# Kernel optimization log

Measured on AMD Instinct MI355X. Metric: run time of the kernel, lower is better.

Reference implementation:

```python
import jax, jax.numpy as jnp
import numpy as np
from jax.scipy.special import logsumexp

B = 2048       # anchors
P = 4          # positives per anchor (constant -> ragged list collapses to [B,P])
D = 256        # embed dim
N_NEG = 32768  # shared negative bank
TEMPERATURE = 0.05
ALPHA = 0.1
EPS = 1e-12    # F.normalize eps


def _l2norm(x):
    n = jnp.sqrt(jnp.sum(x * x, axis=-1, keepdims=True))
    return x / jnp.maximum(n, EPS)


def setup_inputs() -> dict:
    key = jax.random.key(0)
    k1, k2, k3 = jax.random.split(key, 3)
    return {
        "anchor_embeddings": jax.random.normal(k1, (B, D), jnp.float32),
        "positive_embeddings": jax.random.normal(k2, (B * P, D), jnp.float32),
        "negative_embeddings": jax.random.normal(k3, (N_NEG, D), jnp.float32),
        "num_positives_per_anchor": jnp.full((B,), P, dtype=jnp.int32),
    }


def reference(anchor_embeddings, positive_embeddings, negative_embeddings,
              num_positives_per_anchor):
    a = _l2norm(anchor_embeddings)                       # [B, D]
    p = _l2norm(positive_embeddings).reshape(B, P, D)    # [B, P, D]
    n = _l2norm(negative_embeddings)                     # [N, D]

    pos_sim = jnp.einsum("bd,bpd->bp", a, p) / TEMPERATURE   # [B, P]
    neg_sim = jnp.einsum("bd,nd->bn", a, n) / TEMPERATURE    # [B, N]  (dominant traffic)
    neg_lse = logsumexp(neg_sim, axis=1)                     # [B]

    # per-(anchor, positive) CE with label 0 over logits [pos_j, neg_sim_i]:
    # loss = logsumexp([pos_j, neg...]) - pos_j = logaddexp(pos_j, neg_lse_i) - pos_j
    pair_loss = jnp.logaddexp(pos_sim, neg_lse[:, None]) - pos_sim   # [B, P]
    counts = num_positives_per_anchor
    pair_mask = jnp.arange(P)[None, :] < counts[:, None]             # [B, P]
    total = jnp.sum(jnp.where(pair_mask, pair_loss, 0.0))

    # weighted-positive term (only for anchors with num_pos > 1)
    w = jax.nn.softmax(pos_sim, axis=1)                  # [B, P]
    wps = jnp.sum(w * pos_sim, axis=1)                   # [B]
    wloss = jnp.logaddexp(wps, neg_lse) - wps            # [B]
    total = total + ALPHA * jnp.sum(jnp.where(counts > 1, wloss, 0.0))

    return total / B
```

## Files before the change

### kernel.cpp

```cpp
#include <hip/hip_runtime.h>
#include <math.h>

constexpr int   B       = 2048;
constexpr int   P       = 4;
constexpr int   D       = 256;
constexpr int   NNEG    = 32768;
constexpr int   NTILES  = NNEG / 32;
constexpr float TEMP    = 0.05f;
constexpr float ALPHA   = 0.1f;
constexpr float EPS     = 1e-12f;
constexpr float INV_T   = 1.0f / TEMP;
constexpr float SCALE_Q = 28.853900817779268f;

typedef float f32x4 __attribute__((ext_vector_type(4)));
typedef int   i32x8 __attribute__((ext_vector_type(8)));

__device__ inline unsigned short f2bf(float f) {
  unsigned int u = __float_as_uint(f);
  u = (u + 0x7fffu + ((u >> 16) & 1u)) >> 16;
  return (unsigned short)u;
}
__device__ inline float bf2f(unsigned short u) {
  return __uint_as_float((unsigned int)u << 16);
}

__device__ inline float ror16_add(float v) {
  int x;
  x = __builtin_amdgcn_update_dpp(0, __float_as_int(v), 0x121, 0xf, 0xf, true);
  v += __int_as_float(x);
  x = __builtin_amdgcn_update_dpp(0, __float_as_int(v), 0x122, 0xf, 0xf, true);
  v += __int_as_float(x);
  x = __builtin_amdgcn_update_dpp(0, __float_as_int(v), 0x124, 0xf, 0xf, true);
  v += __int_as_float(x);
  x = __builtin_amdgcn_update_dpp(0, __float_as_int(v), 0x128, 0xf, 0xf, true);
  v += __int_as_float(x);
  return v;
}


constexpr int NPANEL = (B + NNEG) / 16;
constexpr int LSTR   = 264;

__global__ __launch_bounds__(256) void prep_kernel(
    const float* __restrict__ a,
    const float* __restrict__ pzx,
    const float* __restrict__ n,
    unsigned char* __restrict__ a_f8,
    unsigned char* __restrict__ n_f8,
    float* __restrict__ pos_sim,
    float* __restrict__ loss_acc,
    unsigned int* __restrict__ ticket) {
  if (blockIdx.x == 0 && threadIdx.x == 0) { *loss_acc = 0.0f; *ticket = 0u; }
  const int id   = blockIdx.x;
  const int tid  = threadIdx.x;
  const int wave = tid >> 6;
  const int lane = tid & 63;

  if (id < NPANEL) {
    __shared__ __align__(16) unsigned short sm[16 * LSTR];
    const bool isA = (id < B / 16);
    const float* src; unsigned char* dst; int prow; float post;
    if (isA) { src = a; dst = a_f8; prow = id;          post = SCALE_Q; }
    else     { src = n; dst = n_f8; prow = id - B / 16; post = 1.0f; }

#pragma unroll
    for (int rr = 0; rr < 4; rr++) {
      const int r = wave * 4 + rr;
      float4 v = ((const float4*)(src + ((size_t)prow * 16 + r) * D))[lane];
      float ss = v.x * v.x + v.y * v.y + v.z * v.z + v.w * v.w;
#pragma unroll
      for (int off = 32; off > 0; off >>= 1) ss += __shfl_xor(ss, off, 64);
      float inv = post / fmaxf(sqrtf(ss), EPS);
      ushort4 o;
      o.x = f2bf(v.x * inv); o.y = f2bf(v.y * inv);
      o.z = f2bf(v.z * inv); o.w = f2bf(v.w * inv);
      *(ushort4*)&sm[r * LSTR + lane * 4] = o;
    }
    __syncthreads();

    const int o = tid * 16;
    int r, k0;
    if (isA) {
      r  = (o >> 4) & 15;
      k0 = (o >> 11) * 128 + ((o >> 8) & 3) * 32 + ((o >> 10) & 1) * 16;
    } else {
      r  = (o >> 5) & 15;
      k0 = (o >> 11) * 128 + ((o >> 9) & 3) * 32 + (o & 16);
    }
    const unsigned short* s1 = &sm[r * LSTR + k0];
    uint4 ov;
    {
      int w0 = __builtin_amdgcn_cvt_pk_fp8_f32(bf2f(s1[0]),  bf2f(s1[1]),  0,  false);
      w0     = __builtin_amdgcn_cvt_pk_fp8_f32(bf2f(s1[2]),  bf2f(s1[3]),  w0, true);
      int w1 = __builtin_amdgcn_cvt_pk_fp8_f32(bf2f(s1[4]),  bf2f(s1[5]),  0,  false);
      w1     = __builtin_amdgcn_cvt_pk_fp8_f32(bf2f(s1[6]),  bf2f(s1[7]),  w1, true);
      int w2 = __builtin_amdgcn_cvt_pk_fp8_f32(bf2f(s1[8]),  bf2f(s1[9]),  0,  false);
      w2     = __builtin_amdgcn_cvt_pk_fp8_f32(bf2f(s1[10]), bf2f(s1[11]), w2, true);
      int w3 = __builtin_amdgcn_cvt_pk_fp8_f32(bf2f(s1[12]), bf2f(s1[13]), 0,  false);
      w3     = __builtin_amdgcn_cvt_pk_fp8_f32(bf2f(s1[14]), bf2f(s1[15]), w3, true);
      ov.x = (unsigned)w0; ov.y = (unsigned)w1;
      ov.z = (unsigned)w2; ov.w = (unsigned)w3;
    }
    *(uint4*)(dst + (size_t)prow * 4096 + tid * 16) = ov;
  } else {
    int pw = (id - NPANEL) * 4 + wave;
    if (pw >= B * P) return;
    int b = pw >> 2;
    float4 av = ((const float4*)(a + (size_t)b * D))[lane];
    float4 pv = ((const float4*)(pzx + (size_t)pw * D))[lane];
    float d  = av.x * pv.x + av.y * pv.y + av.z * pv.z + av.w * pv.w;
    float sa = av.x * av.x + av.y * av.y + av.z * av.z + av.w * av.w;
    float sp = pv.x * pv.x + pv.y * pv.y + pv.z * pv.z + pv.w * pv.w;
#pragma unroll
    for (int off = 32; off > 0; off >>= 1) {
      d  += __shfl_xor(d, off, 64);
      sa += __shfl_xor(sa, off, 64);
      sp += __shfl_xor(sp, off, 64);
    }
    if (lane == 0) {
      float inva = 1.0f / fmaxf(sqrtf(sa), EPS);
      float invp = 1.0f / fmaxf(sqrtf(sp), EPS);
      pos_sim[pw] = d * inva * invp * INV_T;
    }
  }
}

__global__ __launch_bounds__(512, 4) void negsim_mfma_kernel(
    const unsigned char* __restrict__ Af,
    const unsigned char* __restrict__ Nf,
    float* __restrict__ part_s) {
  __shared__ __align__(16) unsigned char As[4 * 4096];

  const int tid  = threadIdx.x;
  const int wave = tid >> 6;
  const int lane = tid & 63;

  const int id     = blockIdx.x;
  const int ngroup = id & 15;
  const int mblk   = id >> 4;
  const int m0     = mblk * 64;

#pragma unroll
  for (int t = 0; t < 2; t++) {
    const int s = wave * 2 + t;
    __builtin_amdgcn_global_load_lds(
        (const __attribute__((address_space(1))) unsigned int*)
            (Af + (size_t)(m0 >> 4) * 4096 + s * 1024 + lane * 16),
        (__attribute__((address_space(3))) unsigned int*)(As + s * 1024 + lane * 16),
        16, 0, 0);
  }

  const unsigned char* Bw = Nf + (size_t)(ngroup * 128 + wave * 2) * 4096 + lane * 32;

  i32x8 bfA0 = *(const i32x8*)(Bw);
  i32x8 bfA1 = *(const i32x8*)(Bw + 4096);

  __syncthreads();

  const int aoff    = lane * 16;
  const int rowbase = m0 + (lane >> 4) * 4;
  const int colbase = ngroup * 64 + wave;

#pragma unroll 1
  for (int it = 0; it < 8; it++) {
    const unsigned char* Bp  = Bw + (size_t)it * 16 * 4096;
    const unsigned char* Bpn = Bw + (size_t)(((it + 1) & 7) * 16) * 4096;

    f32x4 acc[4][2] = {};

    i32x8 bfB0 = *(const i32x8*)(Bp + 2048);
    i32x8 bfB1 = *(const i32x8*)(Bp + 4096 + 2048);
#pragma unroll
    for (int mi = 0; mi < 4; mi++) {
      int4 lo = *(const int4*)&As[mi * 4096 + aoff];
      int4 hi = *(const int4*)&As[mi * 4096 + 1024 + aoff];
      i32x8 af;
      af[0] = lo.x; af[1] = lo.y; af[2] = lo.z; af[3] = lo.w;
      af[4] = hi.x; af[5] = hi.y; af[6] = hi.z; af[7] = hi.w;
      acc[mi][0] = __builtin_amdgcn_mfma_scale_f32_16x16x128_f8f6f4(
          af, bfA0, acc[mi][0], 0, 0, 0, 0x7f7f7f7f, 0, 0x7f7f7f7f);
      acc[mi][1] = __builtin_amdgcn_mfma_scale_f32_16x16x128_f8f6f4(
          af, bfA1, acc[mi][1], 0, 0, 0, 0x7f7f7f7f, 0, 0x7f7f7f7f);
    }

    bfA0 = *(const i32x8*)(Bpn);
    bfA1 = *(const i32x8*)(Bpn + 4096);
#pragma unroll
    for (int mi = 0; mi < 4; mi++) {
      int4 lo = *(const int4*)&As[mi * 4096 + 2048 + aoff];
      int4 hi = *(const int4*)&As[mi * 4096 + 2048 + 1024 + aoff];
      i32x8 af;
      af[0] = lo.x; af[1] = lo.y; af[2] = lo.z; af[3] = lo.w;
      af[4] = hi.x; af[5] = hi.y; af[6] = hi.z; af[7] = hi.w;
      acc[mi][0] = __builtin_amdgcn_mfma_scale_f32_16x16x128_f8f6f4(
          af, bfB0, acc[mi][0], 0, 0, 0, 0x7f7f7f7f, 0, 0x7f7f7f7f);
      acc[mi][1] = __builtin_amdgcn_mfma_scale_f32_16x16x128_f8f6f4(
          af, bfB1, acc[mi][1], 0, 0, 0, 0x7f7f7f7f, 0, 0x7f7f7f7f);
    }

    const int col = colbase + it * 8;
#pragma unroll
    for (int mi = 0; mi < 4; mi++) {
#pragma unroll
      for (int rr = 0; rr < 4; rr++) {
        float e = __builtin_amdgcn_exp2f(acc[mi][0][rr]) +
                  __builtin_amdgcn_exp2f(acc[mi][1][rr]);
        e = ror16_add(e);
        if ((lane & 15) == 0)
          part_s[(size_t)(rowbase + mi * 16 + rr) * NTILES + col] = e;
      }
    }
  }
}

__global__ void loss_kernel(const float* __restrict__ part_s,
                            const float* __restrict__ pos_sim,
                            const int* __restrict__ counts,
                            float* __restrict__ loss_acc,
                            unsigned int* __restrict__ ticket,
                            float* __restrict__ out) {
  const int tid = threadIdx.x;
  const int b   = blockIdx.x * 16 + (tid >> 4);
  const int sub = tid & 15;
  const float* ps = part_s + (size_t)b * NTILES;
  float s = 0.0f;
#pragma unroll
  for (int i = 0; i < NTILES / 16; i++) s += ps[sub + i * 16];
  s += __shfl_xor(s, 1, 64);
  s += __shfl_xor(s, 2, 64);
  s += __shfl_xor(s, 4, 64);
  s += __shfl_xor(s, 8, 64);

  float acc = 0.0f;
  if (sub == 0) {
    float L = logf(s);
    float p0 = pos_sim[b * P + 0], p1 = pos_sim[b * P + 1];
    float p2 = pos_sim[b * P + 2], p3 = pos_sim[b * P + 3];
    int cnt = counts[b];
    float pj[P] = {p0, p1, p2, p3};
#pragma unroll
    for (int jj = 0; jj < P; jj++) {
      if (jj < cnt) {
        float hi = fmaxf(pj[jj], L), lo = fminf(pj[jj], L);
        acc += hi + log1pf(__expf(lo - hi)) - pj[jj];
      }
    }
    float mp = fmaxf(fmaxf(p0, p1), fmaxf(p2, p3));
    float e0 = __expf(p0 - mp), e1 = __expf(p1 - mp);
    float e2 = __expf(p2 - mp), e3 = __expf(p3 - mp);
    float se = e0 + e1 + e2 + e3;
    float wps = (e0 * p0 + e1 * p1 + e2 * p2 + e3 * p3) / se;
    if (cnt > 1) {
      float hi = fmaxf(wps, L), lo = fminf(wps, L);
      acc += ALPHA * (hi + log1pf(__expf(lo - hi)) - wps);
    }
  }
#pragma unroll
  for (int off = 32; off > 0; off >>= 1) acc += __shfl_xor(acc, off, 64);
  __shared__ float sa[4];
  int wid = tid >> 6, lane = tid & 63;
  if (lane == 0) sa[wid] = acc;
  __syncthreads();
  if (tid == 0) {
    atomicAdd(loss_acc, sa[0] + sa[1] + sa[2] + sa[3]);
    __threadfence();
    unsigned int t = atomicAdd(ticket, 1u);
    if (t == (unsigned int)gridDim.x - 1u) {
      float total = atomicAdd(loss_acc, 0.0f);
      out[0] = total / (float)B;
    }
  }
}

extern "C" void kernel_launch(void* const* d_in, const int* in_sizes, int n_in,
                              void* d_out, int out_size, void* d_ws,
                              size_t ws_size, hipStream_t stream) {
  const float* anc    = (const float*)d_in[0];
  const float* pos    = (const float*)d_in[1];
  const float* neg    = (const float*)d_in[2];
  const int*   counts = (const int*)d_in[3];
  float* out = (float*)d_out;

  unsigned char* a_f8 = (unsigned char*)d_ws;
  unsigned char* n_f8 = a_f8 + (size_t)B * D;
  float* part_s  = (float*)(n_f8 + (size_t)NNEG * D);
  float* pos_sim = part_s + (size_t)B * NTILES;
  float* loss_acc = pos_sim + B * P;
  unsigned int* ticket = (unsigned int*)(loss_acc + 1);

  prep_kernel<<<NPANEL + B * P / 4, 256, 0, stream>>>(
      anc, pos, neg, a_f8, n_f8, pos_sim, loss_acc, ticket);

  negsim_mfma_kernel<<<512, 512, 0, stream>>>(a_f8, n_f8, part_s);

  loss_kernel<<<B / 16, 256, 0, stream>>>(part_s, pos_sim, counts,
                                          loss_acc, ticket, out);
}
```

Before: 137.9 us.

## Reduce negsim partials across wave pairs in LDS and deepen B prefetch

Each wave's per-row exp-sum partials are now staged in a double-buffered LDS array, and pairs of waves are summed before the global write. This halves the number of partial tiles (NTILES becomes NNEG/64), which cuts part_s traffic and the work of the loss kernel's reduction. The B-fragment prefetch also changes to fetch a whole iteration ahead: the loop handles two iterations per trip and keeps four fragments per iteration in registers. The cost is a block-wide barrier per iteration and higher register pressure.

Result: faster. 123.9 us (-10.1%).

```diff
diff --git a/kernel.cpp b/kernel.cpp
--- a/kernel.cpp
+++ b/kernel.cpp
@@ -5,7 +5,7 @@
 constexpr int   P       = 4;
 constexpr int   D       = 256;
 constexpr int   NNEG    = 32768;
-constexpr int   NTILES  = NNEG / 32;
+constexpr int   NTILES  = NNEG / 64;
 constexpr float TEMP    = 0.05f;
 constexpr float ALPHA   = 0.1f;
 constexpr float EPS     = 1e-12f;
@@ -130,6 +130,7 @@
     const unsigned char* __restrict__ Nf,
     float* __restrict__ part_s) {
   __shared__ __align__(16) unsigned char As[4 * 4096];
+  __shared__ float part_l[2][8][64];
 
   const int tid  = threadIdx.x;
   const int wave = tid >> 6;
@@ -152,65 +153,87 @@
 
   const unsigned char* Bw = Nf + (size_t)(ngroup * 128 + wave * 2) * 4096 + lane * 32;
 
-  i32x8 bfA0 = *(const i32x8*)(Bw);
-  i32x8 bfA1 = *(const i32x8*)(Bw + 4096);
+  i32x8 bfP0 = *(const i32x8*)(Bw);
+  i32x8 bfP1 = *(const i32x8*)(Bw + 4096);
+  i32x8 bfP2 = *(const i32x8*)(Bw + 2048);
+  i32x8 bfP3 = *(const i32x8*)(Bw + 4096 + 2048);
 
   __syncthreads();
 
-  const int aoff    = lane * 16;
-  const int rowbase = m0 + (lane >> 4) * 4;
-  const int colbase = ngroup * 64 + wave;
+  const int aoff = lane * 16;
+
+#define DO_ITER(B0, B1, B2, B3, PB, ITEXPR)                                    \
+  {                                                                            \
+    f32x4 acc[4][2] = {};                                                      \
+    _Pragma("unroll")                                                          \
+    for (int mi = 0; mi < 4; mi++) {                                           \
+      int4 lo = *(const int4*)&As[mi * 4096 + aoff];                           \
+      int4 hi = *(const int4*)&As[mi * 4096 + 1024 + aoff];                    \
+      i32x8 af;                                                                \
+      af[0] = lo.x; af[1] = lo.y; af[2] = lo.z; af[3] = lo.w;                  \
+      af[4] = hi.x; af[5] = hi.y; af[6] = hi.z; af[7] = hi.w;                  \
+      acc[mi][0] = __builtin_amdgcn_mfma_scale_f32_16x16x128_f8f6f4(           \
+          af, B0, acc[mi][0], 0, 0, 0, 0x7f7f7f7f, 0, 0x7f7f7f7f);             \
+      acc[mi][1] = __builtin_amdgcn_mfma_scale_f32_16x16x128_f8f6f4(           \
+          af, B1, acc[mi][1], 0, 0, 0, 0x7f7f7f7f, 0, 0x7f7f7f7f);             \
+    }                                                                          \
+    _Pragma("unroll")                                                          \
+    for (int mi = 0; mi < 4; mi++) {                                           \
+      int4 lo = *(const int4*)&As[mi * 4096 + 2048 + aoff];                    \
+      int4 hi = *(const int4*)&As[mi * 4096 + 2048 + 1024 + aoff];             \
+      i32x8 af;                                                                \
+      af[0] = lo.x; af[1] = lo.y; af[2] = lo.z; af[3] = lo.w;                  \
+      af[4] = hi.x; af[5] = hi.y; af[6] = hi.z; af[7] = hi.w;                  \
+      acc[mi][0] = __builtin_amdgcn_mfma_scale_f32_16x16x128_f8f6f4(           \
+          af, B2, acc[mi][0], 0, 0, 0, 0x7f7f7f7f, 0, 0x7f7f7f7f);             \
+      acc[mi][1] = __builtin_amdgcn_mfma_scale_f32_16x16x128_f8f6f4(           \
+          af, B3, acc[mi][1], 0, 0, 0, 0x7f7f7f7f, 0, 0x7f7f7f7f);             \
+    }                                                                          \
+    _Pragma("unroll")                                                          \
+    for (int mi = 0; mi < 4; mi++) {                                           \
+      _Pragma("unroll")                                                        \
+      for (int rr = 0; rr < 4; rr++) {                                         \
+        float e = __builtin_amdgcn_exp2f(acc[mi][0][rr]) +                     \
+                  __builtin_amdgcn_exp2f(acc[mi][1][rr]);                      \
+        e = ror16_add(e);                                                      \
+        if ((lane & 15) == 0)                                                  \
+          part_l[PB][wave][mi * 16 + (lane >> 4) * 4 + rr] = e;                \
+      }                                                                        \
+    }                                                                          \
+    asm volatile("s_waitcnt lgkmcnt(0)" ::: "memory");                         \
+    __builtin_amdgcn_sched_barrier(0);                                         \
+    __builtin_amdgcn_s_barrier();                                              \
+    __builtin_amdgcn_sched_barrier(0);                                         \
+    if (tid < 256) {                                                           \
+      const int u4  = tid >> 6;                                                \
+      const int row = tid & 63;                                                \
+      float s64 = part_l[PB][2 * u4][row] + part_l[PB][2 * u4 + 1][row];       \
+      part_s[(size_t)(m0 + row) * NTILES + (ngroup * 32 + (ITEXPR) * 4 + u4)]  \
+          = s64;                                                               \
+    }                                                                          \
+  }
 
 #pragma unroll 1
-  for (int it = 0; it < 8; it++) {
-    const unsigned char* Bp  = Bw + (size_t)it * 16 * 4096;
-    const unsigned char* Bpn = Bw + (size_t)(((it + 1) & 7) * 16) * 4096;
-
-    f32x4 acc[4][2] = {};
-
-    i32x8 bfB0 = *(const i32x8*)(Bp + 2048);
-    i32x8 bfB1 = *(const i32x8*)(Bp + 4096 + 2048);
-#pragma unroll
-    for (int mi = 0; mi < 4; mi++) {
-      int4 lo = *(const int4*)&As[mi * 4096 + aoff];
-      int4 hi = *(const int4*)&As[mi * 4096 + 1024 + aoff];
-      i32x8 af;
-      af[0] = lo.x; af[1] = lo.y; af[2] = lo.z; af[3] = lo.w;
-      af[4] = hi.x; af[5] = hi.y; af[6] = hi.z; af[7] = hi.w;
-      acc[mi][0] = __builtin_amdgcn_mfma_scale_f32_16x16x128_f8f6f4(
-          af, bfA0, acc[mi][0], 0, 0, 0, 0x7f7f7f7f, 0, 0x7f7f7f7f);
-      acc[mi][1] = __builtin_amdgcn_mfma_scale_f32_16x16x128_f8f6f4(
-          af, bfA1, acc[mi][1], 0, 0, 0, 0x7f7f7f7f, 0, 0x7f7f7f7f);
-    }
-
-    bfA0 = *(const i32x8*)(Bpn);
-    bfA1 = *(const i32x8*)(Bpn + 4096);
-#pragma unroll
-    for (int mi = 0; mi < 4; mi++) {
-      int4 lo = *(const int4*)&As[mi * 4096 + 2048 + aoff];
-      int4 hi = *(const int4*)&As[mi * 4096 + 2048 + 1024 + aoff];
-      i32x8 af;
-      af[0] = lo.x; af[1] = lo.y; af[2] = lo.z; af[3] = lo.w;
-      af[4] = hi.x; af[5] = hi.y; af[6] = hi.z; af[7] = hi.w;
-      acc[mi][0] = __builtin_amdgcn_mfma_scale_f32_16x16x128_f8f6f4(
-          af, bfB0, acc[mi][0], 0, 0, 0, 0x7f7f7f7f, 0, 0x7f7f7f7f);
-      acc[mi][1] = __builtin_amdgcn_mfma_scale_f32_16x16x128_f8f6f4(
-          af, bfB1, acc[mi][1], 0, 0, 0, 0x7f7f7f7f, 0, 0x7f7f7f7f);
-    }
-
-    const int col = colbase + it * 8;
-#pragma unroll
-    for (int mi = 0; mi < 4; mi++) {
-#pragma unroll
-      for (int rr = 0; rr < 4; rr++) {
-        float e = __builtin_amdgcn_exp2f(acc[mi][0][rr]) +
-                  __builtin_amdgcn_exp2f(acc[mi][1][rr]);
-        e = ror16_add(e);
-        if ((lane & 15) == 0)
-          part_s[(size_t)(rowbase + mi * 16 + rr) * NTILES + col] = e;
-      }
-    }
-  }
+  for (int t = 0; t < 4; t++) {
+    const int it0 = 2 * t;
+    const unsigned char* Bq  = Bw + (size_t)(it0 + 1) * 16 * 4096;
+    const unsigned char* Bpn = Bw + (size_t)((it0 + 2) & 7) * 16 * 4096;
+
+    i32x8 bfQ0 = *(const i32x8*)(Bq);
+    i32x8 bfQ1 = *(const i32x8*)(Bq + 4096);
+    i32x8 bfQ2 = *(const i32x8*)(Bq + 2048);
+    i32x8 bfQ3 = *(const i32x8*)(Bq + 4096 + 2048);
+
+    DO_ITER(bfP0, bfP1, bfP2, bfP3, 0, it0)
+
+    bfP0 = *(const i32x8*)(Bpn);
+    bfP1 = *(const i32x8*)(Bpn + 4096);
+    bfP2 = *(const i32x8*)(Bpn + 2048);
+    bfP3 = *(const i32x8*)(Bpn + 4096 + 2048);
+
+    DO_ITER(bfQ0, bfQ1, bfQ2, bfQ3, 1, it0 + 1)
+  }
+#undef DO_ITER
 }
 
 __global__ void loss_kernel(const float* __restrict__ part_s,
```
